# Performance work log

Measured on AMD Instinct MI355X. Metric: run time of the kernel, lower is better.

The kernel has to match this reference:

```python
import jax, jax.numpy as jnp
import numpy as np

N_ENTS = 50000
N_EDGES = 500000
N_RELS = 200
RANK = 128
N_LAYERS = 2
RRELU_SLOPE = (1.0 / 8.0 + 1.0 / 3.0) / 2.0  # F.rrelu eval-mode: mean of default lower/upper


def setup_inputs() -> dict:
    key = jax.random.key(0)
    ks = jax.random.split(key, 9)
    return {
        "ent_emb": jax.random.normal(ks[0], (N_ENTS, RANK), dtype=jnp.float32),
        "rel_emb": jax.random.normal(ks[1], (N_RELS, RANK), dtype=jnp.float32),
        "norm": jax.random.uniform(ks[2], (N_ENTS, 1), dtype=jnp.float32),
        "Wn": jax.random.normal(ks[3], (N_LAYERS, RANK, RANK), dtype=jnp.float32) * 0.05,
        "Wl": jax.random.normal(ks[4], (N_LAYERS, RANK, RANK), dtype=jnp.float32) * 0.05,
        "Wa": jax.random.normal(ks[5], (N_LAYERS, RANK, RANK), dtype=jnp.float32) * 0.05,
        "src": jax.random.randint(ks[6], (N_EDGES,), 0, N_ENTS, dtype=jnp.int32),
        "dst": jax.random.randint(ks[7], (N_EDGES,), 0, N_ENTS, dtype=jnp.int32),
        "etype": jax.random.randint(ks[8], (N_EDGES,), 0, N_RELS, dtype=jnp.int32),
    }


def reference(ent_emb, rel_emb, norm, Wn, Wl, Wa, src, dst, etype):
    n = ent_emb.shape[0]
    # in-degree mask (same graph across layers)
    in_deg = jax.ops.segment_sum(jnp.ones_like(dst, dtype=jnp.float32), dst, num_segments=n)
    has_in = (in_deg > 0)[:, None]  # [N,1]
    h = ent_emb
    for l in range(Wn.shape[0]):
        # edge gather + add + linear: msg = (h[src] + rel_emb[etype]) @ Wn[l]
        msg = (h[src] + rel_emb[etype]) @ Wn[l]  # [E, rank]
        # scatter-sum into destination nodes, then per-node norm
        agg = jax.ops.segment_sum(msg, dst, num_segments=n) * norm  # [N, rank]
        # masked self-loop: loop_weight where in_degree>0, else alone_loop_weight
        loop = jnp.where(has_in, h @ Wl[l], h @ Wa[l])
        h = agg + loop
        # rrelu in eval mode == leaky relu with slope (1/8 + 1/3)/2
        h = jnp.where(h >= 0, h, h * RRELU_SLOPE)
        # dropout=0.0 -> identity
    return h
```

## Files before the change

kernel.cpp:

```cpp
#include <hip/hip_runtime.h>

#define SLOPE 0.22916666666666666f
#define ALONE_CAP 2048

typedef __attribute__((ext_vector_type(8))) short bfrag;
typedef __attribute__((ext_vector_type(4))) float ffrag;

__device__ __forceinline__ unsigned short rne16(float f) {
    unsigned u = __float_as_uint(f);
    return (unsigned short)((u + 0x7FFFu + ((u >> 16) & 1u)) >> 16);
}
__device__ __forceinline__ float bf2f(unsigned short h) {
    return __uint_as_float(((unsigned)h) << 16);
}
__device__ __forceinline__ unsigned packsplit(float f) {
    unsigned short hi = rne16(f);
    unsigned short lo = rne16(f - bf2f(hi));
    return ((unsigned)hi << 16) | lo;
}
__device__ __forceinline__ float recon(unsigned u) {
    return __uint_as_float(u & 0xFFFF0000u) + __uint_as_float(u << 16);
}
__device__ __forceinline__ float4 recon4(uint4 u) {
    return make_float4(recon(u.x), recon(u.y), recon(u.z), recon(u.w));
}

__global__ __launch_bounds__(256) void prep_kernel(
    const int* __restrict__ dst, int* __restrict__ deg, int e, int eb,
    const float* __restrict__ ent, unsigned* __restrict__ Esp,
    int total4, int cb,
    const float* __restrict__ Wn, const float* __restrict__ Wl,
    ushort* __restrict__ packW) {
    int b = blockIdx.x;
    if (b < eb) {
        int i = b * 256 + threadIdx.x;
        if (i < e) atomicAdd(&deg[dst[i]], 1);
    } else if (b < eb + cb) {
        int i = (b - eb) * 256 + threadIdx.x;
        if (i >= total4) return;
        float4 v = ((const float4*)ent)[i];
        uint4 w;
        w.x = packsplit(v.x); w.y = packsplit(v.y);
        w.z = packsplit(v.z); w.w = packsplit(v.w);
        ((uint4*)Esp)[i] = w;
    } else {
        int t = (b - eb - cb) * 256 + threadIdx.x;
        if (t >= 4 * 4 * 128 * 4) return;
        int quad = t & 3;
        int nn   = (t >> 2) & 127;
        int kc   = (t >> 9) & 3;
        int mat  = t >> 11;
        const float* W = ((mat & 1) ? Wl : Wn) + (mat >> 1) * 16384;
        ushort* oh = packW + mat * 32768;
        ushort* ol = oh + 16384;
        int obase = kc * 4096 + (nn >> 4) * 512 + (quad * 16 + (nn & 15)) * 8;
        #pragma unroll
        for (int j = 0; j < 8; ++j) {
            float w = W[(kc * 32 + quad * 8 + j) * 128 + nn];
            unsigned short hi = rne16(w);
            oh[obase + j] = hi;
            ol[obase + j] = rne16(w - bf2f(hi));
        }
    }
}

__global__ __launch_bounds__(256) void scan_partial_kernel(const int* __restrict__ deg,
                                                           int* __restrict__ partial, int n) {
    __shared__ int wsum[4];
    int base = blockIdx.x * 1024;
    int t = threadIdx.x;
    int s = 0;
    #pragma unroll
    for (int j = 0; j < 4; ++j) {
        int i = base + t + 256 * j;
        if (i < n) s += deg[i];
    }
    #pragma unroll
    for (int off = 1; off < 64; off <<= 1) s += __shfl_xor(s, off, 64);
    if ((t & 63) == 0) wsum[t >> 6] = s;
    __syncthreads();
    if (t == 0) partial[blockIdx.x] = wsum[0] + wsum[1] + wsum[2] + wsum[3];
}

__global__ __launch_bounds__(256) void scan_final_kernel(const int* __restrict__ deg,
                                                         const int* __restrict__ partial,
                                                         int* __restrict__ row_off,
                                                         int* __restrict__ alone_list,
                                                         int* __restrict__ alone_count, int n) {
    __shared__ int wsum[4];
    __shared__ int sbase;
    int bid = blockIdx.x;
    int t = threadIdx.x, lane = t & 63, wid = t >> 6;
    if (wid == 0) {
        int v = (lane < bid) ? partial[lane] : 0;
        #pragma unroll
        for (int off = 1; off < 64; off <<= 1) v += __shfl_xor(v, off, 64);
        if (lane == 0) sbase = v;
    }
    int base = bid * 1024;
    int i0 = base + t * 4;
    int v0 = (i0 + 0 < n) ? deg[i0 + 0] : 0;
    int v1 = (i0 + 1 < n) ? deg[i0 + 1] : 0;
    int v2 = (i0 + 2 < n) ? deg[i0 + 2] : 0;
    int v3 = (i0 + 3 < n) ? deg[i0 + 3] : 0;
    int s = v0 + v1 + v2 + v3;
    int x = s;
    #pragma unroll
    for (int off = 1; off < 64; off <<= 1) {
        int y = __shfl_up(x, off, 64);
        if (lane >= off) x += y;
    }
    if (lane == 63) wsum[wid] = x;
    __syncthreads();
    int wbase = 0;
    #pragma unroll
    for (int w = 0; w < 4; ++w) { int ws = wsum[w]; if (w < wid) wbase += ws; }
    int p = sbase + wbase + x - s;
    if (i0 + 0 <= n) row_off[i0 + 0] = p;
    p += v0;
    if (i0 + 1 <= n) row_off[i0 + 1] = p;
    p += v1;
    if (i0 + 2 <= n) row_off[i0 + 2] = p;
    p += v2;
    if (i0 + 3 <= n) row_off[i0 + 3] = p;
    if (i0 + 0 < n && v0 == 0) { int q = atomicAdd(alone_count, 1); if (q < ALONE_CAP) alone_list[q] = i0; }
    if (i0 + 1 < n && v1 == 0) { int q = atomicAdd(alone_count, 1); if (q < ALONE_CAP) alone_list[q] = i0 + 1; }
    if (i0 + 2 < n && v2 == 0) { int q = atomicAdd(alone_count, 1); if (q < ALONE_CAP) alone_list[q] = i0 + 2; }
    if (i0 + 3 < n && v3 == 0) { int q = atomicAdd(alone_count, 1); if (q < ALONE_CAP) alone_list[q] = i0 + 3; }
}

__global__ __launch_bounds__(256) void scatter_kernel(
    const int* __restrict__ src, const int* __restrict__ dst,
    const int* __restrict__ ety, const int* __restrict__ row_off,
    int* __restrict__ cursor, unsigned* __restrict__ edges, int e) {
    int i = blockIdx.x * 256 + threadIdx.x;
    if (i < e) {
        int v = dst[i];
        int pos = row_off[v] + atomicAdd(&cursor[v], 1);
        edges[pos] = (unsigned)src[i] | ((unsigned)ety[i] << 16);
    }
}

template <int SPLIT>
__global__ __launch_bounds__(256) void agg_kernel(
    const float* __restrict__ hf, const unsigned* __restrict__ hs,
    const float* __restrict__ rel,
    const float* __restrict__ norm, const int* __restrict__ row_off,
    const unsigned* __restrict__ edges, unsigned* __restrict__ Ssp, int n) {
    int wave = threadIdx.x >> 6, lane = threadIdx.x & 63;
    int v = blockIdx.x * 4 + wave;
    if (v >= n) return;
    int s0 = row_off[v], s1 = row_off[v + 1];
    float nm = norm[v];
    int half = lane >> 5;
    int c4 = (lane & 31) * 4;
    float4 acc = make_float4(0.f, 0.f, 0.f, 0.f);
    int e = s0;
    for (; e + 7 < s1; e += 8) {
        unsigned q0 = edges[e + half];
        unsigned q1 = edges[e + 2 + half];
        unsigned q2 = edges[e + 4 + half];
        unsigned q3 = edges[e + 6 + half];
        float4 h0, h1, h2, h3;
        if (SPLIT) {
            h0 = recon4(*(const uint4*)&hs[(size_t)(q0 & 0xFFFFu) * 128 + c4]);
            h1 = recon4(*(const uint4*)&hs[(size_t)(q1 & 0xFFFFu) * 128 + c4]);
            h2 = recon4(*(const uint4*)&hs[(size_t)(q2 & 0xFFFFu) * 128 + c4]);
            h3 = recon4(*(const uint4*)&hs[(size_t)(q3 & 0xFFFFu) * 128 + c4]);
        } else {
            h0 = *(const float4*)&hf[(size_t)(q0 & 0xFFFFu) * 128 + c4];
            h1 = *(const float4*)&hf[(size_t)(q1 & 0xFFFFu) * 128 + c4];
            h2 = *(const float4*)&hf[(size_t)(q2 & 0xFFFFu) * 128 + c4];
            h3 = *(const float4*)&hf[(size_t)(q3 & 0xFFFFu) * 128 + c4];
        }
        float4 r0 = *(const float4*)&rel[(size_t)(q0 >> 16) * 128 + c4];
        float4 r1 = *(const float4*)&rel[(size_t)(q1 >> 16) * 128 + c4];
        float4 r2 = *(const float4*)&rel[(size_t)(q2 >> 16) * 128 + c4];
        float4 r3 = *(const float4*)&rel[(size_t)(q3 >> 16) * 128 + c4];
        acc.x += ((h0.x + r0.x) + (h1.x + r1.x)) + ((h2.x + r2.x) + (h3.x + r3.x));
        acc.y += ((h0.y + r0.y) + (h1.y + r1.y)) + ((h2.y + r2.y) + (h3.y + r3.y));
        acc.z += ((h0.z + r0.z) + (h1.z + r1.z)) + ((h2.z + r2.z) + (h3.z + r3.z));
        acc.w += ((h0.w + r0.w) + (h1.w + r1.w)) + ((h2.w + r2.w) + (h3.w + r3.w));
    }
    for (; e + 1 < s1; e += 2) {
        unsigned q0 = edges[e + half];
        float4 h0 = SPLIT ? recon4(*(const uint4*)&hs[(size_t)(q0 & 0xFFFFu) * 128 + c4])
                          : *(const float4*)&hf[(size_t)(q0 & 0xFFFFu) * 128 + c4];
        float4 r0 = *(const float4*)&rel[(size_t)(q0 >> 16) * 128 + c4];
        acc.x += h0.x + r0.x; acc.y += h0.y + r0.y;
        acc.z += h0.z + r0.z; acc.w += h0.w + r0.w;
    }
    if (e < s1 && half == 0) {
        unsigned q0 = edges[e];
        float4 h0 = SPLIT ? recon4(*(const uint4*)&hs[(size_t)(q0 & 0xFFFFu) * 128 + c4])
                          : *(const float4*)&hf[(size_t)(q0 & 0xFFFFu) * 128 + c4];
        float4 r0 = *(const float4*)&rel[(size_t)(q0 >> 16) * 128 + c4];
        acc.x += h0.x + r0.x; acc.y += h0.y + r0.y;
        acc.z += h0.z + r0.z; acc.w += h0.w + r0.w;
    }
    acc.x += __shfl_xor(acc.x, 32, 64);
    acc.y += __shfl_xor(acc.y, 32, 64);
    acc.z += __shfl_xor(acc.z, 32, 64);
    acc.w += __shfl_xor(acc.w, 32, 64);
    if (half == 0) {
        uint4 w;
        w.x = packsplit(acc.x * nm); w.y = packsplit(acc.y * nm);
        w.z = packsplit(acc.z * nm); w.w = packsplit(acc.w * nm);
        *(uint4*)&Ssp[(size_t)v * 128 + c4] = w;
    }
}

__global__ __launch_bounds__(256, 2) void gemm_mfma_kernel(
    const unsigned* __restrict__ Ssp, const unsigned* Hsp,
    const ushort* __restrict__ Pnh, const ushort* __restrict__ Pnl,
    const ushort* __restrict__ Plh, const ushort* __restrict__ Pll,
    float* __restrict__ out, unsigned* Osp, int n) {
    __shared__ ushort ldsB[2][2][4096];

    const int tid = threadIdx.x;
    const int wave = tid >> 6, lane = tid & 63;
    const int quad = lane >> 4, l16 = lane & 15;
    const int row_base = blockIdx.x * 64 + wave * 16;

    int r0c = row_base + l16;
    if (r0c > n - 1) r0c = n - 1;
    const size_t arow = (size_t)r0c * 128;
    const int q8 = quad * 8;

    ffrag acc[8];
    #pragma unroll
    for (int ct = 0; ct < 8; ++ct) acc[ct] = (ffrag)0.f;

    uint4 a00 = *(const uint4*)(Ssp + arow + 0 * 32 + q8);
    uint4 a01 = *(const uint4*)(Ssp + arow + 0 * 32 + q8 + 4);
    uint4 a10 = *(const uint4*)(Ssp + arow + 1 * 32 + q8);
    uint4 a11 = *(const uint4*)(Ssp + arow + 1 * 32 + q8 + 4);
    uint4 a20 = *(const uint4*)(Ssp + arow + 2 * 32 + q8);
    uint4 a21 = *(const uint4*)(Ssp + arow + 2 * 32 + q8 + 4);
    uint4 a30 = *(const uint4*)(Ssp + arow + 3 * 32 + q8);
    uint4 a31 = *(const uint4*)(Ssp + arow + 3 * 32 + q8 + 4);
    uint4 a40 = *(const uint4*)(Hsp + arow + 0 * 32 + q8);
    uint4 a41 = *(const uint4*)(Hsp + arow + 0 * 32 + q8 + 4);
    uint4 a50 = *(const uint4*)(Hsp + arow + 1 * 32 + q8);
    uint4 a51 = *(const uint4*)(Hsp + arow + 1 * 32 + q8 + 4);
    uint4 a60 = *(const uint4*)(Hsp + arow + 2 * 32 + q8);
    uint4 a61 = *(const uint4*)(Hsp + arow + 2 * 32 + q8 + 4);
    uint4 a70 = *(const uint4*)(Hsp + arow + 3 * 32 + q8);
    uint4 a71 = *(const uint4*)(Hsp + arow + 3 * 32 + q8 + 4);
    {
        uint4 t0 = *(const uint4*)(Pnh + tid * 8);
        uint4 t1 = *(const uint4*)(Pnh + 2048 + tid * 8);
        uint4 t2 = *(const uint4*)(Pnl + tid * 8);
        uint4 t3 = *(const uint4*)(Pnl + 2048 + tid * 8);
        *(uint4*)&ldsB[0][0][tid * 8] = t0;
        *(uint4*)&ldsB[0][0][2048 + tid * 8] = t1;
        *(uint4*)&ldsB[0][1][tid * 8] = t2;
        *(uint4*)&ldsB[0][1][2048 + tid * 8] = t3;
    }
    __syncthreads();

#define GSTEP(IT, A0, A1, NPH, NPL, NKC, HAVE)                                   \
    {                                                                            \
        uint4 s0, s1, s2, s3;                                                    \
        if (HAVE) {                                                              \
            s0 = *(const uint4*)((NPH) + (NKC) * 4096 + tid * 8);                \
            s1 = *(const uint4*)((NPH) + (NKC) * 4096 + 2048 + tid * 8);         \
            s2 = *(const uint4*)((NPL) + (NKC) * 4096 + tid * 8);                \
            s3 = *(const uint4*)((NPL) + (NKC) * 4096 + 2048 + tid * 8);         \
        }                                                                        \
        bfrag bh[8], bl[8];                                                      \
        _Pragma("unroll")                                                        \
        for (int ct = 0; ct < 8; ++ct) {                                         \
            bh[ct] = *(const bfrag*)&ldsB[(IT) & 1][0][ct * 512 + lane * 8];     \
            bl[ct] = *(const bfrag*)&ldsB[(IT) & 1][1][ct * 512 + lane * 8];     \
        }                                                                        \
        bfrag ah, al;                                                            \
        _Pragma("unroll")                                                        \
        for (int j = 0; j < 4; ++j) {                                            \
            unsigned u0 = ((const unsigned*)&(A0))[j];                           \
            unsigned u1 = ((const unsigned*)&(A1))[j];                           \
            ah[j]     = (short)(u0 >> 16); al[j]     = (short)(u0 & 0xFFFFu);    \
            ah[j + 4] = (short)(u1 >> 16); al[j + 4] = (short)(u1 & 0xFFFFu);    \
        }                                                                        \
        _Pragma("unroll")                                                        \
        for (int ct = 0; ct < 8; ++ct)                                           \
            acc[ct] = __builtin_amdgcn_mfma_f32_16x16x32_bf16(ah, bh[ct], acc[ct], 0, 0, 0); \
        _Pragma("unroll")                                                        \
        for (int ct = 0; ct < 8; ++ct)                                           \
            acc[ct] = __builtin_amdgcn_mfma_f32_16x16x32_bf16(ah, bl[ct], acc[ct], 0, 0, 0); \
        _Pragma("unroll")                                                        \
        for (int ct = 0; ct < 8; ++ct)                                           \
            acc[ct] = __builtin_amdgcn_mfma_f32_16x16x32_bf16(al, bh[ct], acc[ct], 0, 0, 0); \
        if (HAVE) {                                                              \
            *(uint4*)&ldsB[((IT) + 1) & 1][0][tid * 8] = s0;                     \
            *(uint4*)&ldsB[((IT) + 1) & 1][0][2048 + tid * 8] = s1;              \
            *(uint4*)&ldsB[((IT) + 1) & 1][1][tid * 8] = s2;                     \
            *(uint4*)&ldsB[((IT) + 1) & 1][1][2048 + tid * 8] = s3;              \
            __syncthreads();                                                     \
        }                                                                        \
    }

    GSTEP(0, a00, a01, Pnh, Pnl, 1, 1)
    GSTEP(1, a10, a11, Pnh, Pnl, 2, 1)
    GSTEP(2, a20, a21, Pnh, Pnl, 3, 1)
    GSTEP(3, a30, a31, Plh, Pll, 0, 1)
    GSTEP(4, a40, a41, Plh, Pll, 1, 1)
    GSTEP(5, a50, a51, Plh, Pll, 2, 1)
    GSTEP(6, a60, a61, Plh, Pll, 3, 1)
    GSTEP(7, a70, a71, Plh, Pll, 0, 0)
#undef GSTEP

    #pragma unroll
    for (int ct = 0; ct < 8; ++ct) {
        #pragma unroll
        for (int rg = 0; rg < 4; ++rg) {
            int r = row_base + quad * 4 + rg;
            if (r < n) {
                int c = ct * 16 + l16;
                float v = acc[ct][rg];
                v = v >= 0.f ? v : v * SLOPE;
                if (out) out[(size_t)r * 128 + c] = v;
                if (Osp) Osp[(size_t)r * 128 + c] = packsplit(v);
            }
        }
    }
}

__global__ __launch_bounds__(128) void fixup_kernel(
    const float* __restrict__ Hrows, int by_node,
    const float* __restrict__ Wa,
    const int* __restrict__ alone_list, const int* __restrict__ alone_count,
    float* out, unsigned* Osp, float* asave) {
    int cnt = *alone_count;
    if (cnt > ALONE_CAP) cnt = ALONE_CAP;
    int t = threadIdx.x;
    for (int i = blockIdx.x; i < cnt; i += gridDim.x) {
        int v = alone_list[i];
        const float* hrow = Hrows + (size_t)(by_node ? v : i) * 128;
        float acc = 0.f;
        for (int k = 0; k < 128; ++k)
            acc += hrow[k] * Wa[k * 128 + t];
        float o = acc >= 0.f ? acc : acc * SLOPE;
        if (out) out[(size_t)v * 128 + t] = o;
        if (Osp) Osp[(size_t)v * 128 + t] = packsplit(o);
        if (asave) asave[(size_t)i * 128 + t] = o;
    }
}

extern "C" void kernel_launch(void* const* d_in, const int* in_sizes, int n_in,
                              void* d_out, int out_size, void* d_ws, size_t ws_size,
                              hipStream_t stream) {
    const float* ent  = (const float*)d_in[0];
    const float* rel  = (const float*)d_in[1];
    const float* norm = (const float*)d_in[2];
    const float* Wn   = (const float*)d_in[3];
    const float* Wl   = (const float*)d_in[4];
    const float* Wa   = (const float*)d_in[5];
    const int*   src  = (const int*)d_in[6];
    const int*   dst  = (const int*)d_in[7];
    const int*   ety  = (const int*)d_in[8];
    float* out = (float*)d_out;

    const int n = in_sizes[2];
    const int e = in_sizes[7];

    char* ws = (char*)d_ws;
    int* deg         = (int*)ws;
    int* cursor      = deg + n;
    int* alone_count = cursor + n;
    size_t zbytes = (size_t)(2 * n + 1) * sizeof(int);
    size_t p = (zbytes + 255) & ~(size_t)255;
    int* row_off = (int*)(ws + p);
    p += (((size_t)(n + 1) * 4) + 255) & ~(size_t)255;
    int* partial = (int*)(ws + p);
    p += 256;
    int* alone_list = (int*)(ws + p);
    p += (((size_t)ALONE_CAP * 4) + 255) & ~(size_t)255;
    float* asave = (float*)(ws + p);
    p += (((size_t)ALONE_CAP * 128 * 4) + 255) & ~(size_t)255;
    unsigned* edges = (unsigned*)(ws + p);
    p += (((size_t)e * 4) + 255) & ~(size_t)255;
    unsigned* Ssp = (unsigned*)(ws + p);
    p += (((size_t)n * 128 * 4) + 255) & ~(size_t)255;
    unsigned* Esp = (unsigned*)(ws + p);
    p += (((size_t)n * 128 * 4) + 255) & ~(size_t)255;
    ushort* packW = (ushort*)(ws + p);
    p += 4 * 32768 * 2;

    const int eb = (e + 255) / 256;
    const int cb = (n * 32 + 255) / 256;
    const int nparts = (n + 1023) / 1024;
    const int gb = (n + 63) / 64;
    const int ab = (n + 3) / 4;

    hipMemsetAsync(ws, 0, zbytes, stream);
    prep_kernel<<<eb + cb + 32, 256, 0, stream>>>(dst, deg, e, eb,
                                                  ent, Esp, n * 32, cb,
                                                  Wn, Wl, packW);
    scan_partial_kernel<<<nparts, 256, 0, stream>>>(deg, partial, n);
    scan_final_kernel<<<nparts, 256, 0, stream>>>(deg, partial, row_off,
                                                  alone_list, alone_count, n);
    scatter_kernel<<<eb, 256, 0, stream>>>(src, dst, ety, row_off, cursor, edges, e);

    agg_kernel<0><<<ab, 256, 0, stream>>>(ent, nullptr, rel, norm, row_off, edges, Ssp, n);
    gemm_mfma_kernel<<<gb, 256, 0, stream>>>(Ssp, Esp,
                                             packW, packW + 16384,
                                             packW + 32768, packW + 49152,
                                             nullptr, Esp, n);
    fixup_kernel<<<16, 128, 0, stream>>>(ent, 1, Wa, alone_list, alone_count,
                                         nullptr, Esp, asave);

    agg_kernel<1><<<ab, 256, 0, stream>>>(nullptr, Esp, rel, norm, row_off, edges, Ssp, n);
    gemm_mfma_kernel<<<gb, 256, 0, stream>>>(Ssp, Esp,
                                             packW + 65536, packW + 81920,
                                             packW + 98304, packW + 114688,
                                             out, nullptr, n);
    fixup_kernel<<<16, 128, 0, stream>>>(asave, 0, Wa + 16384, alone_list, alone_count,
                                         out, nullptr, nullptr);
}
```

Baseline: 282.5 us.

## Fuse edge aggregation into the MFMA GEMM kernel through an LDS staging tile

```diff
diff --git a/kernel.cpp b/kernel.cpp
--- a/kernel.cpp
+++ b/kernel.cpp
@@ -142,79 +142,15 @@
 }
 
 template <int SPLIT>
-__global__ __launch_bounds__(256) void agg_kernel(
-    const float* __restrict__ hf, const unsigned* __restrict__ hs,
-    const float* __restrict__ rel,
-    const float* __restrict__ norm, const int* __restrict__ row_off,
-    const unsigned* __restrict__ edges, unsigned* __restrict__ Ssp, int n) {
-    int wave = threadIdx.x >> 6, lane = threadIdx.x & 63;
-    int v = blockIdx.x * 4 + wave;
-    if (v >= n) return;
-    int s0 = row_off[v], s1 = row_off[v + 1];
-    float nm = norm[v];
-    int half = lane >> 5;
-    int c4 = (lane & 31) * 4;
-    float4 acc = make_float4(0.f, 0.f, 0.f, 0.f);
-    int e = s0;
-    for (; e + 7 < s1; e += 8) {
-        unsigned q0 = edges[e + half];
-        unsigned q1 = edges[e + 2 + half];
-        unsigned q2 = edges[e + 4 + half];
-        unsigned q3 = edges[e + 6 + half];
-        float4 h0, h1, h2, h3;
-        if (SPLIT) {
-            h0 = recon4(*(const uint4*)&hs[(size_t)(q0 & 0xFFFFu) * 128 + c4]);
-            h1 = recon4(*(const uint4*)&hs[(size_t)(q1 & 0xFFFFu) * 128 + c4]);
-            h2 = recon4(*(const uint4*)&hs[(size_t)(q2 & 0xFFFFu) * 128 + c4]);
-            h3 = recon4(*(const uint4*)&hs[(size_t)(q3 & 0xFFFFu) * 128 + c4]);
-        } else {
-            h0 = *(const float4*)&hf[(size_t)(q0 & 0xFFFFu) * 128 + c4];
-            h1 = *(const float4*)&hf[(size_t)(q1 & 0xFFFFu) * 128 + c4];
-            h2 = *(const float4*)&hf[(size_t)(q2 & 0xFFFFu) * 128 + c4];
-            h3 = *(const float4*)&hf[(size_t)(q3 & 0xFFFFu) * 128 + c4];
-        }
-        float4 r0 = *(const float4*)&rel[(size_t)(q0 >> 16) * 128 + c4];
-        float4 r1 = *(const float4*)&rel[(size_t)(q1 >> 16) * 128 + c4];
-        float4 r2 = *(const float4*)&rel[(size_t)(q2 >> 16) * 128 + c4];
-        float4 r3 = *(const float4*)&rel[(size_t)(q3 >> 16) * 128 + c4];
-        acc.x += ((h0.x + r0.x) + (h1.x + r1.x)) + ((h2.x + r2.x) + (h3.x + r3.x));
-        acc.y += ((h0.y + r0.y) + (h1.y + r1.y)) + ((h2.y + r2.y) + (h3.y + r3.y));
-        acc.z += ((h0.z + r0.z) + (h1.z + r1.z)) + ((h2.z + r2.z) + (h3.z + r3.z));
-        acc.w += ((h0.w + r0.w) + (h1.w + r1.w)) + ((h2.w + r2.w) + (h3.w + r3.w));
-    }
-    for (; e + 1 < s1; e += 2) {
-        unsigned q0 = edges[e + half];
-        float4 h0 = SPLIT ? recon4(*(const uint4*)&hs[(size_t)(q0 & 0xFFFFu) * 128 + c4])
-                          : *(const float4*)&hf[(size_t)(q0 & 0xFFFFu) * 128 + c4];
-        float4 r0 = *(const float4*)&rel[(size_t)(q0 >> 16) * 128 + c4];
-        acc.x += h0.x + r0.x; acc.y += h0.y + r0.y;
-        acc.z += h0.z + r0.z; acc.w += h0.w + r0.w;
-    }
-    if (e < s1 && half == 0) {
-        unsigned q0 = edges[e];
-        float4 h0 = SPLIT ? recon4(*(const uint4*)&hs[(size_t)(q0 & 0xFFFFu) * 128 + c4])
-                          : *(const float4*)&hf[(size_t)(q0 & 0xFFFFu) * 128 + c4];
-        float4 r0 = *(const float4*)&rel[(size_t)(q0 >> 16) * 128 + c4];
-        acc.x += h0.x + r0.x; acc.y += h0.y + r0.y;
-        acc.z += h0.z + r0.z; acc.w += h0.w + r0.w;
-    }
-    acc.x += __shfl_xor(acc.x, 32, 64);
-    acc.y += __shfl_xor(acc.y, 32, 64);
-    acc.z += __shfl_xor(acc.z, 32, 64);
-    acc.w += __shfl_xor(acc.w, 32, 64);
-    if (half == 0) {
-        uint4 w;
-        w.x = packsplit(acc.x * nm); w.y = packsplit(acc.y * nm);
-        w.z = packsplit(acc.z * nm); w.w = packsplit(acc.w * nm);
-        *(uint4*)&Ssp[(size_t)v * 128 + c4] = w;
-    }
-}
-
-__global__ __launch_bounds__(256, 2) void gemm_mfma_kernel(
-    const unsigned* __restrict__ Ssp, const unsigned* Hsp,
+__global__ __launch_bounds__(256, 2) void fused_layer_kernel(
+    const float* __restrict__ gf, const unsigned* __restrict__ gs,
+    const unsigned* __restrict__ Hsp,
+    const float* __restrict__ rel, const float* __restrict__ norm,
+    const int* __restrict__ row_off, const unsigned* __restrict__ edges,
     const ushort* __restrict__ Pnh, const ushort* __restrict__ Pnl,
     const ushort* __restrict__ Plh, const ushort* __restrict__ Pll,
-    float* __restrict__ out, unsigned* Osp, int n) {
+    float* out, unsigned* Osp, int n) {
+    __shared__ float Sld[64][132];
     __shared__ ushort ldsB[2][2][4096];
 
     const int tid = threadIdx.x;
@@ -227,26 +163,14 @@
     const size_t arow = (size_t)r0c * 128;
     const int q8 = quad * 8;
 
-    ffrag acc[8];
-    #pragma unroll
-    for (int ct = 0; ct < 8; ++ct) acc[ct] = (ffrag)0.f;
-
-    uint4 a00 = *(const uint4*)(Ssp + arow + 0 * 32 + q8);
-    uint4 a01 = *(const uint4*)(Ssp + arow + 0 * 32 + q8 + 4);
-    uint4 a10 = *(const uint4*)(Ssp + arow + 1 * 32 + q8);
-    uint4 a11 = *(const uint4*)(Ssp + arow + 1 * 32 + q8 + 4);
-    uint4 a20 = *(const uint4*)(Ssp + arow + 2 * 32 + q8);
-    uint4 a21 = *(const uint4*)(Ssp + arow + 2 * 32 + q8 + 4);
-    uint4 a30 = *(const uint4*)(Ssp + arow + 3 * 32 + q8);
-    uint4 a31 = *(const uint4*)(Ssp + arow + 3 * 32 + q8 + 4);
-    uint4 a40 = *(const uint4*)(Hsp + arow + 0 * 32 + q8);
-    uint4 a41 = *(const uint4*)(Hsp + arow + 0 * 32 + q8 + 4);
-    uint4 a50 = *(const uint4*)(Hsp + arow + 1 * 32 + q8);
-    uint4 a51 = *(const uint4*)(Hsp + arow + 1 * 32 + q8 + 4);
-    uint4 a60 = *(const uint4*)(Hsp + arow + 2 * 32 + q8);
-    uint4 a61 = *(const uint4*)(Hsp + arow + 2 * 32 + q8 + 4);
-    uint4 a70 = *(const uint4*)(Hsp + arow + 3 * 32 + q8);
-    uint4 a71 = *(const uint4*)(Hsp + arow + 3 * 32 + q8 + 4);
+    uint4 h00 = *(const uint4*)(Hsp + arow + 0 * 32 + q8);
+    uint4 h01 = *(const uint4*)(Hsp + arow + 0 * 32 + q8 + 4);
+    uint4 h10 = *(const uint4*)(Hsp + arow + 1 * 32 + q8);
+    uint4 h11 = *(const uint4*)(Hsp + arow + 1 * 32 + q8 + 4);
+    uint4 h20 = *(const uint4*)(Hsp + arow + 2 * 32 + q8);
+    uint4 h21 = *(const uint4*)(Hsp + arow + 2 * 32 + q8 + 4);
+    uint4 h30 = *(const uint4*)(Hsp + arow + 3 * 32 + q8);
+    uint4 h31 = *(const uint4*)(Hsp + arow + 3 * 32 + q8 + 4);
     {
         uint4 t0 = *(const uint4*)(Pnh + tid * 8);
         uint4 t1 = *(const uint4*)(Pnh + 2048 + tid * 8);
@@ -257,23 +181,134 @@
         *(uint4*)&ldsB[0][1][tid * 8] = t2;
         *(uint4*)&ldsB[0][1][2048 + tid * 8] = t3;
     }
+
+    {
+        const int half = lane >> 5;
+        const int c4 = (lane & 31) * 4;
+        #pragma unroll 1
+        for (int i = 0; i < 16; ++i) {
+            const int v = row_base + i;
+            float4 acc = make_float4(0.f, 0.f, 0.f, 0.f);
+            float nm = 0.f;
+            if (v < n) {
+                nm = norm[v];
+                int s0 = row_off[v], s1 = row_off[v + 1];
+                int e = s0;
+                for (; e + 7 < s1; e += 8) {
+                    unsigned q0 = edges[e + half];
+                    unsigned q1 = edges[e + 2 + half];
+                    unsigned q2 = edges[e + 4 + half];
+                    unsigned q3 = edges[e + 6 + half];
+                    float4 h0, h1, h2, h3;
+                    if (SPLIT) {
+                        h0 = recon4(*(const uint4*)&gs[(size_t)(q0 & 0xFFFFu) * 128 + c4]);
+                        h1 = recon4(*(const uint4*)&gs[(size_t)(q1 & 0xFFFFu) * 128 + c4]);
+                        h2 = recon4(*(const uint4*)&gs[(size_t)(q2 & 0xFFFFu) * 128 + c4]);
+                        h3 = recon4(*(const uint4*)&gs[(size_t)(q3 & 0xFFFFu) * 128 + c4]);
+                    } else {
+                        h0 = *(const float4*)&gf[(size_t)(q0 & 0xFFFFu) * 128 + c4];
+                        h1 = *(const float4*)&gf[(size_t)(q1 & 0xFFFFu) * 128 + c4];
+                        h2 = *(const float4*)&gf[(size_t)(q2 & 0xFFFFu) * 128 + c4];
+                        h3 = *(const float4*)&gf[(size_t)(q3 & 0xFFFFu) * 128 + c4];
+                    }
+                    float4 r0 = *(const float4*)&rel[(size_t)(q0 >> 16) * 128 + c4];
+                    float4 r1 = *(const float4*)&rel[(size_t)(q1 >> 16) * 128 + c4];
+                    float4 r2 = *(const float4*)&rel[(size_t)(q2 >> 16) * 128 + c4];
+                    float4 r3 = *(const float4*)&rel[(size_t)(q3 >> 16) * 128 + c4];
+                    acc.x += ((h0.x + r0.x) + (h1.x + r1.x)) + ((h2.x + r2.x) + (h3.x + r3.x));
+                    acc.y += ((h0.y + r0.y) + (h1.y + r1.y)) + ((h2.y + r2.y) + (h3.y + r3.y));
+                    acc.z += ((h0.z + r0.z) + (h1.z + r1.z)) + ((h2.z + r2.z) + (h3.z + r3.z));
+                    acc.w += ((h0.w + r0.w) + (h1.w + r1.w)) + ((h2.w + r2.w) + (h3.w + r3.w));
+                }
+                for (; e + 1 < s1; e += 2) {
+                    unsigned q0 = edges[e + half];
+                    float4 h0 = SPLIT ? recon4(*(const uint4*)&gs[(size_t)(q0 & 0xFFFFu) * 128 + c4])
+                                      : *(const float4*)&gf[(size_t)(q0 & 0xFFFFu) * 128 + c4];
+                    float4 r0 = *(const float4*)&rel[(size_t)(q0 >> 16) * 128 + c4];
+                    acc.x += h0.x + r0.x; acc.y += h0.y + r0.y;
+                    acc.z += h0.z + r0.z; acc.w += h0.w + r0.w;
+                }
+                if (e < s1 && half == 0) {
+                    unsigned q0 = edges[e];
+                    float4 h0 = SPLIT ? recon4(*(const uint4*)&gs[(size_t)(q0 & 0xFFFFu) * 128 + c4])
+                                      : *(const float4*)&gf[(size_t)(q0 & 0xFFFFu) * 128 + c4];
+                    float4 r0 = *(const float4*)&rel[(size_t)(q0 >> 16) * 128 + c4];
+                    acc.x += h0.x + r0.x; acc.y += h0.y + r0.y;
+                    acc.z += h0.z + r0.z; acc.w += h0.w + r0.w;
+                }
+            }
+            acc.x += __shfl_xor(acc.x, 32, 64);
+            acc.y += __shfl_xor(acc.y, 32, 64);
+            acc.z += __shfl_xor(acc.z, 32, 64);
+            acc.w += __shfl_xor(acc.w, 32, 64);
+            if (half == 0) {
+                *(float4*)&Sld[wave * 16 + i][c4] =
+                    make_float4(acc.x * nm, acc.y * nm, acc.z * nm, acc.w * nm);
+            }
+        }
+    }
     __syncthreads();
 
-#define GSTEP(IT, A0, A1, NPH, NPL, NKC, HAVE)                                   \
-    {                                                                            \
-        uint4 s0, s1, s2, s3;                                                    \
-        if (HAVE) {                                                              \
-            s0 = *(const uint4*)((NPH) + (NKC) * 4096 + tid * 8);                \
-            s1 = *(const uint4*)((NPH) + (NKC) * 4096 + 2048 + tid * 8);         \
-            s2 = *(const uint4*)((NPL) + (NKC) * 4096 + tid * 8);                \
-            s3 = *(const uint4*)((NPL) + (NKC) * 4096 + 2048 + tid * 8);         \
-        }                                                                        \
+    ffrag acc[8];
+    #pragma unroll
+    for (int ct = 0; ct < 8; ++ct) acc[ct] = (ffrag)0.f;
+
+#define GSTAGE(NPH, NPL, NKC)                                                    \
+        s0 = *(const uint4*)((NPH) + (NKC) * 4096 + tid * 8);                    \
+        s1 = *(const uint4*)((NPH) + (NKC) * 4096 + 2048 + tid * 8);             \
+        s2 = *(const uint4*)((NPL) + (NKC) * 4096 + tid * 8);                    \
+        s3 = *(const uint4*)((NPL) + (NKC) * 4096 + 2048 + tid * 8);
+
+#define GCOMPUTE(IT)                                                             \
         bfrag bh[8], bl[8];                                                      \
         _Pragma("unroll")                                                        \
         for (int ct = 0; ct < 8; ++ct) {                                         \
             bh[ct] = *(const bfrag*)&ldsB[(IT) & 1][0][ct * 512 + lane * 8];     \
             bl[ct] = *(const bfrag*)&ldsB[(IT) & 1][1][ct * 512 + lane * 8];     \
         }                                                                        \
+        _Pragma("unroll")                                                        \
+        for (int ct = 0; ct < 8; ++ct)                                           \
+            acc[ct] = __builtin_amdgcn_mfma_f32_16x16x32_bf16(ah, bh[ct], acc[ct], 0, 0, 0); \
+        _Pragma("unroll")                                                        \
+        for (int ct = 0; ct < 8; ++ct)                                           \
+            acc[ct] = __builtin_amdgcn_mfma_f32_16x16x32_bf16(ah, bl[ct], acc[ct], 0, 0, 0); \
+        _Pragma("unroll")                                                        \
+        for (int ct = 0; ct < 8; ++ct)                                           \
+            acc[ct] = __builtin_amdgcn_mfma_f32_16x16x32_bf16(al, bh[ct], acc[ct], 0, 0, 0);
+
+#define GFINISH(IT, HAVE)                                                        \
+        if (HAVE) {                                                              \
+            *(uint4*)&ldsB[((IT) + 1) & 1][0][tid * 8] = s0;                     \
+            *(uint4*)&ldsB[((IT) + 1) & 1][0][2048 + tid * 8] = s1;              \
+            *(uint4*)&ldsB[((IT) + 1) & 1][1][tid * 8] = s2;                     \
+            *(uint4*)&ldsB[((IT) + 1) & 1][1][2048 + tid * 8] = s3;              \
+            __syncthreads();                                                     \
+        }
+
+#define GSTEP_S(IT, KC, NPH, NPL, NKC, HAVE)                                     \
+    {                                                                            \
+        uint4 s0, s1, s2, s3;                                                    \
+        if (HAVE) { GSTAGE(NPH, NPL, NKC) }                                      \
+        float4 f0 = *(const float4*)&Sld[wave * 16 + l16][(KC) * 32 + q8];       \
+        float4 f1 = *(const float4*)&Sld[wave * 16 + l16][(KC) * 32 + q8 + 4];   \
+        bfrag ah, al;                                                            \
+        _Pragma("unroll")                                                        \
+        for (int j = 0; j < 4; ++j) {                                            \
+            float fa = ((const float*)&f0)[j];                                   \
+            float fb = ((const float*)&f1)[j];                                   \
+            unsigned short ha = rne16(fa);                                       \
+            unsigned short hb = rne16(fb);                                       \
+            ah[j]     = (short)ha; al[j]     = (short)rne16(fa - bf2f(ha));      \
+            ah[j + 4] = (short)hb; al[j + 4] = (short)rne16(fb - bf2f(hb));      \
+        }                                                                        \
+        GCOMPUTE(IT)                                                             \
+        GFINISH(IT, HAVE)                                                        \
+    }
+
+#define GSTEP_H(IT, A0, A1, NPH, NPL, NKC, HAVE)                                 \
+    {                                                                            \
+        uint4 s0, s1, s2, s3;                                                    \
+        if (HAVE) { GSTAGE(NPH, NPL, NKC) }                                      \
         bfrag ah, al;                                                            \
         _Pragma("unroll")                                                        \
         for (int j = 0; j < 4; ++j) {                                            \
@@ -282,33 +317,23 @@
             ah[j]     = (short)(u0 >> 16); al[j]     = (short)(u0 & 0xFFFFu);    \
             ah[j + 4] = (short)(u1 >> 16); al[j + 4] = (short)(u1 & 0xFFFFu);    \
         }                                                                        \
-        _Pragma("unroll")                                                        \
-        for (int ct = 0; ct < 8; ++ct)                                           \
-            acc[ct] = __builtin_amdgcn_mfma_f32_16x16x32_bf16(ah, bh[ct], acc[ct], 0, 0, 0); \
-        _Pragma("unroll")                                                        \
-        for (int ct = 0; ct < 8; ++ct)                                           \
-            acc[ct] = __builtin_amdgcn_mfma_f32_16x16x32_bf16(ah, bl[ct], acc[ct], 0, 0, 0); \
-        _Pragma("unroll")                                                        \
-        for (int ct = 0; ct < 8; ++ct)                                           \
-            acc[ct] = __builtin_amdgcn_mfma_f32_16x16x32_bf16(al, bh[ct], acc[ct], 0, 0, 0); \
-        if (HAVE) {                                                              \
-            *(uint4*)&ldsB[((IT) + 1) & 1][0][tid * 8] = s0;                     \
-            *(uint4*)&ldsB[((IT) + 1) & 1][0][2048 + tid * 8] = s1;              \
-            *(uint4*)&ldsB[((IT) + 1) & 1][1][tid * 8] = s2;                     \
-            *(uint4*)&ldsB[((IT) + 1) & 1][1][2048 + tid * 8] = s3;              \
-            __syncthreads();                                                     \
-        }                                                                        \
-    }
-
-    GSTEP(0, a00, a01, Pnh, Pnl, 1, 1)
-    GSTEP(1, a10, a11, Pnh, Pnl, 2, 1)
-    GSTEP(2, a20, a21, Pnh, Pnl, 3, 1)
-    GSTEP(3, a30, a31, Plh, Pll, 0, 1)
-    GSTEP(4, a40, a41, Plh, Pll, 1, 1)
-    GSTEP(5, a50, a51, Plh, Pll, 2, 1)
-    GSTEP(6, a60, a61, Plh, Pll, 3, 1)
-    GSTEP(7, a70, a71, Plh, Pll, 0, 0)
-#undef GSTEP
+        GCOMPUTE(IT)                                                             \
+        GFINISH(IT, HAVE)                                                        \
+    }
+
+    GSTEP_S(0, 0, Pnh, Pnl, 1, 1)
+    GSTEP_S(1, 1, Pnh, Pnl, 2, 1)
+    GSTEP_S(2, 2, Pnh, Pnl, 3, 1)
+    GSTEP_S(3, 3, Plh, Pll, 0, 1)
+    GSTEP_H(4, h00, h01, Plh, Pll, 1, 1)
+    GSTEP_H(5, h10, h11, Plh, Pll, 2, 1)
+    GSTEP_H(6, h20, h21, Plh, Pll, 3, 1)
+    GSTEP_H(7, h30, h31, Plh, Pll, 0, 0)
+#undef GSTEP_S
+#undef GSTEP_H
+#undef GSTAGE
+#undef GCOMPUTE
+#undef GFINISH
 
     #pragma unroll
     for (int ct = 0; ct < 8; ++ct) {
@@ -380,8 +405,6 @@
     p += (((size_t)ALONE_CAP * 128 * 4) + 255) & ~(size_t)255;
     unsigned* edges = (unsigned*)(ws + p);
     p += (((size_t)e * 4) + 255) & ~(size_t)255;
-    unsigned* Ssp = (unsigned*)(ws + p);
-    p += (((size_t)n * 128 * 4) + 255) & ~(size_t)255;
     unsigned* Esp = (unsigned*)(ws + p);
     p += (((size_t)n * 128 * 4) + 255) & ~(size_t)255;
     ushort* packW = (ushort*)(ws + p);
@@ -391,7 +414,6 @@
     const int cb = (n * 32 + 255) / 256;
     const int nparts = (n + 1023) / 1024;
     const int gb = (n + 63) / 64;
-    const int ab = (n + 3) / 4;
 
     hipMemsetAsync(ws, 0, zbytes, stream);
     prep_kernel<<<eb + cb + 32, 256, 0, stream>>>(dst, deg, e, eb,
@@ -402,19 +424,17 @@
                                                   alone_list, alone_count, n);
     scatter_kernel<<<eb, 256, 0, stream>>>(src, dst, ety, row_off, cursor, edges, e);
 
-    agg_kernel<0><<<ab, 256, 0, stream>>>(ent, nullptr, rel, norm, row_off, edges, Ssp, n);
-    gemm_mfma_kernel<<<gb, 256, 0, stream>>>(Ssp, Esp,
-                                             packW, packW + 16384,
-                                             packW + 32768, packW + 49152,
-                                             nullptr, Esp, n);
+    fused_layer_kernel<0><<<gb, 256, 0, stream>>>(
+        ent, nullptr, Esp, rel, norm, row_off, edges,
+        packW, packW + 16384, packW + 32768, packW + 49152,
+        nullptr, Esp, n);
     fixup_kernel<<<16, 128, 0, stream>>>(ent, 1, Wa, alone_list, alone_count,
                                          nullptr, Esp, asave);
 
-    agg_kernel<1><<<ab, 256, 0, stream>>>(nullptr, Esp, rel, norm, row_off, edges, Ssp, n);
-    gemm_mfma_kernel<<<gb, 256, 0, stream>>>(Ssp, Esp,
-                                             packW + 65536, packW + 81920,
-                                             packW + 98304, packW + 114688,
-                                             out, nullptr, n);
+    fused_layer_kernel<1><<<gb, 256, 0, stream>>>(
+        nullptr, Esp, Esp, rel, norm, row_off, edges,
+        packW + 65536, packW + 81920, packW + 98304, packW + 114688,
+        out, nullptr, n);
     fixup_kernel<<<16, 128, 0, stream>>>(asave, 0, Wa + 16384, alone_list, alone_count,
                                          out, nullptr, nullptr);
 }
```

New measurement: 357.0 us. 26.4% more time.

## Stage whole weight matrices in LDS to cut per-step barriers

Applied to the files above, without the earlier changes.

```diff
diff --git a/kernel.cpp b/kernel.cpp
--- a/kernel.cpp
+++ b/kernel.cpp
@@ -215,7 +215,7 @@
     const ushort* __restrict__ Pnh, const ushort* __restrict__ Pnl,
     const ushort* __restrict__ Plh, const ushort* __restrict__ Pll,
     float* __restrict__ out, unsigned* Osp, int n) {
-    __shared__ ushort ldsB[2][2][4096];
+    __shared__ ushort ldsB[4][2][4096];
 
     const int tid = threadIdx.x;
     const int wave = tid >> 6, lane = tid & 63;
@@ -231,48 +231,49 @@
     #pragma unroll
     for (int ct = 0; ct < 8; ++ct) acc[ct] = (ffrag)0.f;
 
-    uint4 a00 = *(const uint4*)(Ssp + arow + 0 * 32 + q8);
-    uint4 a01 = *(const uint4*)(Ssp + arow + 0 * 32 + q8 + 4);
-    uint4 a10 = *(const uint4*)(Ssp + arow + 1 * 32 + q8);
-    uint4 a11 = *(const uint4*)(Ssp + arow + 1 * 32 + q8 + 4);
-    uint4 a20 = *(const uint4*)(Ssp + arow + 2 * 32 + q8);
-    uint4 a21 = *(const uint4*)(Ssp + arow + 2 * 32 + q8 + 4);
-    uint4 a30 = *(const uint4*)(Ssp + arow + 3 * 32 + q8);
-    uint4 a31 = *(const uint4*)(Ssp + arow + 3 * 32 + q8 + 4);
-    uint4 a40 = *(const uint4*)(Hsp + arow + 0 * 32 + q8);
-    uint4 a41 = *(const uint4*)(Hsp + arow + 0 * 32 + q8 + 4);
-    uint4 a50 = *(const uint4*)(Hsp + arow + 1 * 32 + q8);
-    uint4 a51 = *(const uint4*)(Hsp + arow + 1 * 32 + q8 + 4);
-    uint4 a60 = *(const uint4*)(Hsp + arow + 2 * 32 + q8);
-    uint4 a61 = *(const uint4*)(Hsp + arow + 2 * 32 + q8 + 4);
-    uint4 a70 = *(const uint4*)(Hsp + arow + 3 * 32 + q8);
-    uint4 a71 = *(const uint4*)(Hsp + arow + 3 * 32 + q8 + 4);
-    {
-        uint4 t0 = *(const uint4*)(Pnh + tid * 8);
-        uint4 t1 = *(const uint4*)(Pnh + 2048 + tid * 8);
-        uint4 t2 = *(const uint4*)(Pnl + tid * 8);
-        uint4 t3 = *(const uint4*)(Pnl + 2048 + tid * 8);
-        *(uint4*)&ldsB[0][0][tid * 8] = t0;
-        *(uint4*)&ldsB[0][0][2048 + tid * 8] = t1;
-        *(uint4*)&ldsB[0][1][tid * 8] = t2;
-        *(uint4*)&ldsB[0][1][2048 + tid * 8] = t3;
-    }
-    __syncthreads();
-
-#define GSTEP(IT, A0, A1, NPH, NPL, NKC, HAVE)                                   \
+#define STAGE_MAT(PH, PL)                                                        \
     {                                                                            \
-        uint4 s0, s1, s2, s3;                                                    \
-        if (HAVE) {                                                              \
-            s0 = *(const uint4*)((NPH) + (NKC) * 4096 + tid * 8);                \
-            s1 = *(const uint4*)((NPH) + (NKC) * 4096 + 2048 + tid * 8);         \
-            s2 = *(const uint4*)((NPL) + (NKC) * 4096 + tid * 8);                \
-            s3 = *(const uint4*)((NPL) + (NKC) * 4096 + 2048 + tid * 8);         \
-        }                                                                        \
+        uint4 t00 = *(const uint4*)((PH) + 0 * 4096 + tid * 8);                  \
+        uint4 t01 = *(const uint4*)((PH) + 0 * 4096 + 2048 + tid * 8);           \
+        uint4 t02 = *(const uint4*)((PL) + 0 * 4096 + tid * 8);                  \
+        uint4 t03 = *(const uint4*)((PL) + 0 * 4096 + 2048 + tid * 8);           \
+        uint4 t10 = *(const uint4*)((PH) + 1 * 4096 + tid * 8);                  \
+        uint4 t11 = *(const uint4*)((PH) + 1 * 4096 + 2048 + tid * 8);           \
+        uint4 t12 = *(const uint4*)((PL) + 1 * 4096 + tid * 8);                  \
+        uint4 t13 = *(const uint4*)((PL) + 1 * 4096 + 2048 + tid * 8);           \
+        uint4 t20 = *(const uint4*)((PH) + 2 * 4096 + tid * 8);                  \
+        uint4 t21 = *(const uint4*)((PH) + 2 * 4096 + 2048 + tid * 8);           \
+        uint4 t22 = *(const uint4*)((PL) + 2 * 4096 + tid * 8);                  \
+        uint4 t23 = *(const uint4*)((PL) + 2 * 4096 + 2048 + tid * 8);           \
+        uint4 t30 = *(const uint4*)((PH) + 3 * 4096 + tid * 8);                  \
+        uint4 t31 = *(const uint4*)((PH) + 3 * 4096 + 2048 + tid * 8);           \
+        uint4 t32 = *(const uint4*)((PL) + 3 * 4096 + tid * 8);                  \
+        uint4 t33 = *(const uint4*)((PL) + 3 * 4096 + 2048 + tid * 8);           \
+        *(uint4*)&ldsB[0][0][tid * 8] = t00;                                     \
+        *(uint4*)&ldsB[0][0][2048 + tid * 8] = t01;                              \
+        *(uint4*)&ldsB[0][1][tid * 8] = t02;                                     \
+        *(uint4*)&ldsB[0][1][2048 + tid * 8] = t03;                              \
+        *(uint4*)&ldsB[1][0][tid * 8] = t10;                                     \
+        *(uint4*)&ldsB[1][0][2048 + tid * 8] = t11;                              \
+        *(uint4*)&ldsB[1][1][tid * 8] = t12;                                     \
+        *(uint4*)&ldsB[1][1][2048 + tid * 8] = t13;                              \
+        *(uint4*)&ldsB[2][0][tid * 8] = t20;                                     \
+        *(uint4*)&ldsB[2][0][2048 + tid * 8] = t21;                              \
+        *(uint4*)&ldsB[2][1][tid * 8] = t22;                                     \
+        *(uint4*)&ldsB[2][1][2048 + tid * 8] = t23;                              \
+        *(uint4*)&ldsB[3][0][tid * 8] = t30;                                     \
+        *(uint4*)&ldsB[3][0][2048 + tid * 8] = t31;                              \
+        *(uint4*)&ldsB[3][1][tid * 8] = t32;                                     \
+        *(uint4*)&ldsB[3][1][2048 + tid * 8] = t33;                              \
+    }
+
+#define GSTEP(KC, A0, A1)                                                        \
+    {                                                                            \
         bfrag bh[8], bl[8];                                                      \
         _Pragma("unroll")                                                        \
         for (int ct = 0; ct < 8; ++ct) {                                         \
-            bh[ct] = *(const bfrag*)&ldsB[(IT) & 1][0][ct * 512 + lane * 8];     \
-            bl[ct] = *(const bfrag*)&ldsB[(IT) & 1][1][ct * 512 + lane * 8];     \
+            bh[ct] = *(const bfrag*)&ldsB[KC][0][ct * 512 + lane * 8];           \
+            bl[ct] = *(const bfrag*)&ldsB[KC][1][ct * 512 + lane * 8];           \
         }                                                                        \
         bfrag ah, al;                                                            \
         _Pragma("unroll")                                                        \
@@ -291,24 +292,43 @@
         _Pragma("unroll")                                                        \
         for (int ct = 0; ct < 8; ++ct)                                           \
             acc[ct] = __builtin_amdgcn_mfma_f32_16x16x32_bf16(al, bh[ct], acc[ct], 0, 0, 0); \
-        if (HAVE) {                                                              \
-            *(uint4*)&ldsB[((IT) + 1) & 1][0][tid * 8] = s0;                     \
-            *(uint4*)&ldsB[((IT) + 1) & 1][0][2048 + tid * 8] = s1;              \
-            *(uint4*)&ldsB[((IT) + 1) & 1][1][tid * 8] = s2;                     \
-            *(uint4*)&ldsB[((IT) + 1) & 1][1][2048 + tid * 8] = s3;              \
-            __syncthreads();                                                     \
-        }                                                                        \
-    }
-
-    GSTEP(0, a00, a01, Pnh, Pnl, 1, 1)
-    GSTEP(1, a10, a11, Pnh, Pnl, 2, 1)
-    GSTEP(2, a20, a21, Pnh, Pnl, 3, 1)
-    GSTEP(3, a30, a31, Plh, Pll, 0, 1)
-    GSTEP(4, a40, a41, Plh, Pll, 1, 1)
-    GSTEP(5, a50, a51, Plh, Pll, 2, 1)
-    GSTEP(6, a60, a61, Plh, Pll, 3, 1)
-    GSTEP(7, a70, a71, Plh, Pll, 0, 0)
+    }
+
+    uint4 a00 = *(const uint4*)(Ssp + arow + 0 * 32 + q8);
+    uint4 a01 = *(const uint4*)(Ssp + arow + 0 * 32 + q8 + 4);
+    uint4 a10 = *(const uint4*)(Ssp + arow + 1 * 32 + q8);
+    uint4 a11 = *(const uint4*)(Ssp + arow + 1 * 32 + q8 + 4);
+    uint4 a20 = *(const uint4*)(Ssp + arow + 2 * 32 + q8);
+    uint4 a21 = *(const uint4*)(Ssp + arow + 2 * 32 + q8 + 4);
+    uint4 a30 = *(const uint4*)(Ssp + arow + 3 * 32 + q8);
+    uint4 a31 = *(const uint4*)(Ssp + arow + 3 * 32 + q8 + 4);
+    STAGE_MAT(Pnh, Pnl)
+    __syncthreads();
+
+    GSTEP(0, a00, a01)
+    GSTEP(1, a10, a11)
+    GSTEP(2, a20, a21)
+    GSTEP(3, a30, a31)
+
+    __syncthreads();
+
+    uint4 a40 = *(const uint4*)(Hsp + arow + 0 * 32 + q8);
+    uint4 a41 = *(const uint4*)(Hsp + arow + 0 * 32 + q8 + 4);
+    uint4 a50 = *(const uint4*)(Hsp + arow + 1 * 32 + q8);
+    uint4 a51 = *(const uint4*)(Hsp + arow + 1 * 32 + q8 + 4);
+    uint4 a60 = *(const uint4*)(Hsp + arow + 2 * 32 + q8);
+    uint4 a61 = *(const uint4*)(Hsp + arow + 2 * 32 + q8 + 4);
+    uint4 a70 = *(const uint4*)(Hsp + arow + 3 * 32 + q8);
+    uint4 a71 = *(const uint4*)(Hsp + arow + 3 * 32 + q8 + 4);
+    STAGE_MAT(Plh, Pll)
+    __syncthreads();
+
+    GSTEP(0, a40, a41)
+    GSTEP(1, a50, a51)
+    GSTEP(2, a60, a61)
+    GSTEP(3, a70, a71)
 #undef GSTEP
+#undef STAGE_MAT
 
     #pragma unroll
     for (int ct = 0; ct < 8; ++ct) {
```

After: 276.3 us. -2.2%, faster.
